# Performance work log

Hardware: AMD Instinct MI355X
Metric: run time of the kernel (lower is better)

Reference implementation:

```python
import jax, jax.numpy as jnp
import numpy as np

IN_F, OUT_F = 4096, 11008
MAXQ = 15  # 2**4 - 1 for wbits=4


def setup_inputs() -> dict:
    key = jax.random.key(0)
    k1, k2, k3, k4, k5 = jax.random.split(key, 5)
    inp = jax.random.normal(k1, (4, 64, IN_F), dtype=jnp.float32)
    weight = jax.random.normal(k2, (OUT_F, IN_F), dtype=jnp.float32) * 0.02
    bias = jax.random.normal(k3, (OUT_F,), dtype=jnp.float32) * 0.02
    # per-channel asymmetric quant params (as Quantizer.find_params would produce)
    scale = jax.random.uniform(k4, (OUT_F, 1), dtype=jnp.float32) * 0.01 + 1e-4
    zero = jnp.round(jax.random.uniform(k5, (OUT_F, 1), dtype=jnp.float32) * MAXQ)
    return {"input": inp, "weight": weight, "bias": bias,
            "scale": scale, "zero": zero, "maxq": MAXQ}


def reference(input, weight, bias, scale, zero, maxq):
    # fake-quantize weight: q = clamp(round(w/scale) + zero, 0, maxq); w_dq = scale*(q - zero)
    q = jnp.clip(jnp.round(weight / scale) + zero, 0.0, float(maxq))
    w_dq = scale * (q - zero)                      # [out, in]
    # F.linear: input @ w_dq.T + bias
    out = jnp.einsum('bsi,oi->bso', input, w_dq) + bias
    return out
```

## Files before the change

### kernel.cpp

```cpp
#include <hip/hip_runtime.h>
#include <hip/hip_bf16.h>
#include <stdint.h>

#define K_TOT 4096
#define N_TOT 11008
#define M_TOT 256
#define BM 128
#define BN 64
#define WST 72

using bf16x8 = __attribute__((ext_vector_type(8))) short;
using f32x4  = __attribute__((ext_vector_type(4))) float;

__global__ void cvt_a_bf16(const float* __restrict__ in, uint32_t* __restrict__ out) {
    int i = blockIdx.x * blockDim.x + threadIdx.x;
    const float4 v = ((const float4*)in)[i];
    uint32_t a = __float_as_uint(v.x), b = __float_as_uint(v.y),
             c = __float_as_uint(v.z), d = __float_as_uint(v.w);
    a += 0x7FFFu + ((a >> 16) & 1u);
    b += 0x7FFFu + ((b >> 16) & 1u);
    c += 0x7FFFu + ((c >> 16) & 1u);
    d += 0x7FFFu + ((d >> 16) & 1u);
    uint2 o;
    o.x = (a >> 16) | (b & 0xFFFF0000u);
    o.y = (c >> 16) | (d & 0xFFFF0000u);
    ((uint2*)out)[i] = o;
}

__device__ __forceinline__ void dequant16(const float4 w[4], float rs, float zp, float sc,
                                          uint32_t o[8]) {
    float f[16];
#pragma unroll
    for (int j = 0; j < 4; ++j) {
        f[4 * j + 0] = w[j].x; f[4 * j + 1] = w[j].y;
        f[4 * j + 2] = w[j].z; f[4 * j + 3] = w[j].w;
    }
    uint32_t u[16];
#pragma unroll
    for (int i = 0; i < 16; ++i) {
        float q = rintf(f[i] * rs) + zp;
        q = fminf(fmaxf(q, 0.0f), 15.0f);
        float dq = (q - zp) * sc;
        uint32_t b = __float_as_uint(dq);
        u[i] = b + 0x7FFFu + ((b >> 16) & 1u);
    }
#pragma unroll
    for (int i = 0; i < 8; ++i)
        o[i] = (u[2 * i] >> 16) | (u[2 * i + 1] & 0xFFFF0000u);
}

__device__ __forceinline__ void compute_step(f32x4 acc[4][2], const uint16_t* const Ap[4],
                                             const uint16_t (*sw)[WST], int kt, int wn, int lane) {
    const int koff = kt * 64;
#pragma unroll
    for (int s = 0; s < 2; ++s) {
        bf16x8 a[4], b[2];
#pragma unroll
        for (int mi = 0; mi < 4; ++mi)
            a[mi] = *(const bf16x8*)(Ap[mi] + koff + s * 32);
#pragma unroll
        for (int ni = 0; ni < 2; ++ni)
            b[ni] = *(const bf16x8*)&sw[wn + ni * 16 + (lane & 15)][s * 32 + (lane >> 4) * 8];
#pragma unroll
        for (int mi = 0; mi < 4; ++mi)
#pragma unroll
            for (int ni = 0; ni < 2; ++ni)
                acc[mi][ni] = __builtin_amdgcn_mfma_f32_16x16x32_bf16(a[mi], b[ni], acc[mi][ni], 0, 0, 0);
    }
}

__global__ __launch_bounds__(256, 2)
void wql_gemm(const uint16_t* __restrict__ A,
              const float* __restrict__ W,
              const float* __restrict__ bias,
              const float* __restrict__ scale,
              const float* __restrict__ zero,
              float* __restrict__ O) {
    __shared__ uint16_t sW[2][BN][WST];

    const int tid  = threadIdx.x;
    const int lane = tid & 63;
    const int wv   = tid >> 6;
    const int wm   = (wv & 1) * 64;
    const int wn   = (wv >> 1) * 32;
    const int m0   = blockIdx.x * BM;
    const int n0   = blockIdx.y * BN;

    const int nloc = tid >> 2;
    const int kseg = tid & 3;
    const int wrow = n0 + nloc;
    const float* Wp = W + (size_t)wrow * K_TOT + kseg * 16;
    const float sc = scale[wrow];
    const float zp = zero[wrow];
    const float rs = 1.0f / sc;
    uint16_t* sdst0 = &sW[0][nloc][kseg * 16];
    uint16_t* sdst1 = &sW[1][nloc][kseg * 16];

    const uint16_t* Ap[4];
#pragma unroll
    for (int mi = 0; mi < 4; ++mi)
        Ap[mi] = A + (size_t)(m0 + wm + mi * 16 + (lane & 15)) * K_TOT + (lane >> 4) * 8;

    f32x4 acc[4][2];
#pragma unroll
    for (int mi = 0; mi < 4; ++mi)
#pragma unroll
        for (int ni = 0; ni < 2; ++ni)
            acc[mi][ni] = (f32x4){0.f, 0.f, 0.f, 0.f};

    float4 bank0[4], bank1[4];

#pragma unroll
    for (int j = 0; j < 4; ++j) bank0[j] = ((const float4*)Wp)[j];
    {
        uint32_t o[8];
        dequant16(bank0, rs, zp, sc, o);
        ((uint4*)sdst0)[0] = make_uint4(o[0], o[1], o[2], o[3]);
        ((uint4*)sdst0)[1] = make_uint4(o[4], o[5], o[6], o[7]);
    }
#pragma unroll
    for (int j = 0; j < 4; ++j) bank1[j] = ((const float4*)(Wp + 64))[j];
    __syncthreads();

    for (int kt = 0; kt < K_TOT / 64; kt += 2) {
        if (kt + 2 < 64) {
            const float4* p = (const float4*)(Wp + (size_t)(kt + 2) * 64);
#pragma unroll
            for (int j = 0; j < 4; ++j) bank0[j] = p[j];
        }
        compute_step(acc, Ap, sW[0], kt, wn, lane);
        {
            uint32_t o[8];
            dequant16(bank1, rs, zp, sc, o);
            ((uint4*)sdst1)[0] = make_uint4(o[0], o[1], o[2], o[3]);
            ((uint4*)sdst1)[1] = make_uint4(o[4], o[5], o[6], o[7]);
        }
        __syncthreads();

        if (kt + 3 < 64) {
            const float4* p = (const float4*)(Wp + (size_t)(kt + 3) * 64);
#pragma unroll
            for (int j = 0; j < 4; ++j) bank1[j] = p[j];
        }
        compute_step(acc, Ap, sW[1], kt + 1, wn, lane);
        if (kt + 2 < 64) {
            uint32_t o[8];
            dequant16(bank0, rs, zp, sc, o);
            ((uint4*)sdst0)[0] = make_uint4(o[0], o[1], o[2], o[3]);
            ((uint4*)sdst0)[1] = make_uint4(o[4], o[5], o[6], o[7]);
        }
        __syncthreads();
    }

    const int colbase = n0 + wn + (lane & 15);
    const float bv0 = bias[colbase];
    const float bv1 = bias[colbase + 16];
    const int rbase = m0 + wm + ((lane >> 4) << 2);
#pragma unroll
    for (int mi = 0; mi < 4; ++mi) {
#pragma unroll
        for (int ni = 0; ni < 2; ++ni) {
            const float bv = ni ? bv1 : bv0;
            const int col = colbase + ni * 16;
#pragma unroll
            for (int r = 0; r < 4; ++r) {
                const int row = rbase + mi * 16 + r;
                O[(size_t)row * N_TOT + col] = acc[mi][ni][r] + bv;
            }
        }
    }
}

extern "C" void kernel_launch(void* const* d_in, const int* in_sizes, int n_in,
                              void* d_out, int out_size, void* d_ws, size_t ws_size,
                              hipStream_t stream) {
    const float* inp    = (const float*)d_in[0];
    const float* weight = (const float*)d_in[1];
    const float* bias   = (const float*)d_in[2];
    const float* scale  = (const float*)d_in[3];
    const float* zero   = (const float*)d_in[4];

    uint32_t* Abf = (uint32_t*)d_ws;

    cvt_a_bf16<<<dim3((M_TOT * K_TOT / 4) / 256), dim3(256), 0, stream>>>(inp, Abf);

    dim3 grid(M_TOT / BM, N_TOT / BN);
    wql_gemm<<<grid, dim3(256), 0, stream>>>((const uint16_t*)Abf, weight, bias, scale, zero,
                                             (float*)d_out);
}
```

Measured before the change: 401.8 us.

## Split GEMM along K into partial slices with separate bias-reduction kernel

Adds a split-K dimension to the grid (up to 4 slices, depending on workspace size). Each slice accumulates a partial product over its share of K and writes it to a workspace buffer, and a new reduce kernel sums the slices and adds the bias. The aim is more blocks in flight, since the base grid of 2x172 blocks underfills the GPU, and the launch-bounds occupancy hint is raised accordingly. The cost is extra global traffic for the partial outputs (about 11 MB per slice), an additional kernel launch, and duplicate A and weight-row loads per slice. When the workspace is too small it falls back to one slice, with the reduce pass still run in place on the output.

```diff
diff --git a/kernel.cpp b/kernel.cpp
--- a/kernel.cpp
+++ b/kernel.cpp
@@ -69,13 +69,13 @@
     }
 }
 
-__global__ __launch_bounds__(256, 2)
+__global__ __launch_bounds__(256, 4)
 void wql_gemm(const uint16_t* __restrict__ A,
               const float* __restrict__ W,
-              const float* __restrict__ bias,
               const float* __restrict__ scale,
               const float* __restrict__ zero,
-              float* __restrict__ O) {
+              float* __restrict__ P,
+              int kloc) {
     __shared__ uint16_t sW[2][BN][WST];
 
     const int tid  = threadIdx.x;
@@ -85,11 +85,13 @@
     const int wn   = (wv >> 1) * 32;
     const int m0   = blockIdx.x * BM;
     const int n0   = blockIdx.y * BN;
+    const int k0   = blockIdx.z * kloc;
+    const int nkt  = kloc / 64;
 
     const int nloc = tid >> 2;
     const int kseg = tid & 3;
     const int wrow = n0 + nloc;
-    const float* Wp = W + (size_t)wrow * K_TOT + kseg * 16;
+    const float* Wp = W + (size_t)wrow * K_TOT + k0 + kseg * 16;
     const float sc = scale[wrow];
     const float zp = zero[wrow];
     const float rs = 1.0f / sc;
@@ -99,7 +101,7 @@
     const uint16_t* Ap[4];
 #pragma unroll
     for (int mi = 0; mi < 4; ++mi)
-        Ap[mi] = A + (size_t)(m0 + wm + mi * 16 + (lane & 15)) * K_TOT + (lane >> 4) * 8;
+        Ap[mi] = A + (size_t)(m0 + wm + mi * 16 + (lane & 15)) * K_TOT + k0 + (lane >> 4) * 8;
 
     f32x4 acc[4][2];
 #pragma unroll
@@ -122,8 +124,8 @@
     for (int j = 0; j < 4; ++j) bank1[j] = ((const float4*)(Wp + 64))[j];
     __syncthreads();
 
-    for (int kt = 0; kt < K_TOT / 64; kt += 2) {
-        if (kt + 2 < 64) {
+    for (int kt = 0; kt < nkt; kt += 2) {
+        if (kt + 2 < nkt) {
             const float4* p = (const float4*)(Wp + (size_t)(kt + 2) * 64);
 #pragma unroll
             for (int j = 0; j < 4; ++j) bank0[j] = p[j];
@@ -137,13 +139,13 @@
         }
         __syncthreads();
 
-        if (kt + 3 < 64) {
+        if (kt + 3 < nkt) {
             const float4* p = (const float4*)(Wp + (size_t)(kt + 3) * 64);
 #pragma unroll
             for (int j = 0; j < 4; ++j) bank1[j] = p[j];
         }
         compute_step(acc, Ap, sW[1], kt + 1, wn, lane);
-        if (kt + 2 < 64) {
+        if (kt + 2 < nkt) {
             uint32_t o[8];
             dequant16(bank0, rs, zp, sc, o);
             ((uint4*)sdst0)[0] = make_uint4(o[0], o[1], o[2], o[3]);
@@ -152,23 +154,36 @@
         __syncthreads();
     }
 
+    float* Pb = P + (size_t)blockIdx.z * M_TOT * N_TOT;
     const int colbase = n0 + wn + (lane & 15);
-    const float bv0 = bias[colbase];
-    const float bv1 = bias[colbase + 16];
     const int rbase = m0 + wm + ((lane >> 4) << 2);
 #pragma unroll
     for (int mi = 0; mi < 4; ++mi) {
 #pragma unroll
         for (int ni = 0; ni < 2; ++ni) {
-            const float bv = ni ? bv1 : bv0;
             const int col = colbase + ni * 16;
 #pragma unroll
             for (int r = 0; r < 4; ++r) {
                 const int row = rbase + mi * 16 + r;
-                O[(size_t)row * N_TOT + col] = acc[mi][ni][r] + bv;
+                Pb[(size_t)row * N_TOT + col] = acc[mi][ni][r];
             }
         }
     }
+}
+
+__global__ void reduce_bias(const float* __restrict__ P, const float* __restrict__ bias,
+                            float* __restrict__ out, int ks) {
+    const int i4 = blockIdx.x * blockDim.x + threadIdx.x;
+    const size_t tot4 = (size_t)M_TOT * N_TOT / 4;
+    const int col = (int)(((size_t)i4 * 4) % N_TOT);
+    float4 acc = ((const float4*)P)[i4];
+    for (int s = 1; s < ks; ++s) {
+        const float4 v = ((const float4*)P)[(size_t)s * tot4 + i4];
+        acc.x += v.x; acc.y += v.y; acc.z += v.z; acc.w += v.w;
+    }
+    const float4 b = *(const float4*)(bias + col);
+    acc.x += b.x; acc.y += b.y; acc.z += b.z; acc.w += b.w;
+    ((float4*)out)[i4] = acc;
 }
 
 extern "C" void kernel_launch(void* const* d_in, const int* in_sizes, int n_in,
@@ -180,11 +195,22 @@
     const float* scale  = (const float*)d_in[3];
     const float* zero   = (const float*)d_in[4];
 
+    const size_t A_BYTES = (size_t)M_TOT * K_TOT * 2;
+    const size_t SLICE   = (size_t)M_TOT * N_TOT * 4;
+
     uint32_t* Abf = (uint32_t*)d_ws;
+    float* partial;
+    int KS;
+    if (ws_size >= A_BYTES + 4 * SLICE) { KS = 4; partial = (float*)((char*)d_ws + A_BYTES); }
+    else if (ws_size >= A_BYTES + 2 * SLICE) { KS = 2; partial = (float*)((char*)d_ws + A_BYTES); }
+    else { KS = 1; partial = (float*)d_out; }
 
     cvt_a_bf16<<<dim3((M_TOT * K_TOT / 4) / 256), dim3(256), 0, stream>>>(inp, Abf);
 
-    dim3 grid(M_TOT / BM, N_TOT / BN);
-    wql_gemm<<<grid, dim3(256), 0, stream>>>((const uint16_t*)Abf, weight, bias, scale, zero,
-                                             (float*)d_out);
-}
+    dim3 grid(M_TOT / BM, N_TOT / BN, KS);
+    wql_gemm<<<grid, dim3(256), 0, stream>>>((const uint16_t*)Abf, weight, scale, zero,
+                                             partial, K_TOT / KS);
+
+    reduce_bias<<<dim3((M_TOT * N_TOT / 4) / 256), dim3(256), 0, stream>>>(
+        partial, bias, (float*)d_out, KS);
+}
```

Measured after the change: 368.8 us. 8.2% less time.
